# Optimization experiments

Measured on AMD Instinct MI355X. Metric: run time of the kernel, lower is better.

The kernel has to match this reference:

```python
import jax, jax.numpy as jnp
import numpy as np

QC = 12          # effective quantum channels (quantum_channels//4*4)
G = 3            # number of 4-channel quantum groups
DIM = 128
NGROUPS_GN = 8
NUM_LAYER = 1

# PauliZ sign table: wire 0 is the most-significant qubit (PennyLane default.qubit)
_SIGNS = np.array([[1.0 - 2.0 * ((k >> (3 - w)) & 1) for w in range(4)]
                   for k in range(16)], dtype=np.float32)


def _apply_rx(state, phi, w):
    # state: [B,2,2,2,2] complex64; phi: [B]; RX = cos(p/2) I - i sin(p/2) X
    c = jnp.cos(0.5 * phi).astype(jnp.complex64)
    s = (-1j) * jnp.sin(0.5 * phi).astype(jnp.complex64)
    U = jnp.stack([jnp.stack([c, s], -1), jnp.stack([s, c], -1)], -2)  # [B,2,2]
    st = jnp.moveaxis(state, 1 + w, -1)
    st = jnp.einsum('bij,b...j->b...i', U, st)
    return jnp.moveaxis(st, -1, 1 + w)


def _apply_cnot(state, c, t):
    st = jnp.moveaxis(state, (1 + c, 1 + t), (-2, -1))
    st = jnp.concatenate([st[..., 0:1, :], st[..., 1:2, ::-1]], axis=-2)
    return jnp.moveaxis(st, (-2, -1), (1 + c, 1 + t))


def _circuit(x4, theta):
    # AngleEmbedding(RX) + NUM_LAYER x Basic_ansatz; x4: [B,4], theta: [4*NUM_LAYER]
    B = x4.shape[0]
    state = jnp.zeros((B, 2, 2, 2, 2), jnp.complex64).at[:, 0, 0, 0, 0].set(1.0)
    for w in range(4):
        state = _apply_rx(state, x4[:, w], w)
    for l in range(NUM_LAYER):
        th = theta[4 * l:4 * (l + 1)]
        for w in range(4):
            state = _apply_rx(state, jnp.broadcast_to(th[w], (B,)), w)
        for c in range(3):
            state = _apply_cnot(state, c, c + 1)
        state = _apply_cnot(state, 3, 0)
    probs = jnp.abs(state.reshape(B, 16)) ** 2
    return probs @ jnp.asarray(_SIGNS)  # [B,4] PauliZ expvals


def _quantum_block(x_q, qparams):
    # x_q: [B,H,W,QC]; pool spatially, run per-group circuit, broadcast back
    B, H, W, Cq = x_q.shape
    pooled = jnp.mean(x_q, axis=(1, 2)).reshape(B, Cq // 4, 4)
    y = jax.vmap(_circuit, in_axes=(1, 0), out_axes=1)(pooled, qparams)  # [B,G,4]
    y = y.reshape(B, 1, 1, Cq)
    return jnp.broadcast_to(y, (B, H, W, Cq))


def _ws_conv(x, kernel, bias):
    eps = 1e-5  # fp32 branch of WeightStandardizedConv
    mean = jnp.mean(kernel, axis=(0, 1, 2), keepdims=True)
    var = jnp.var(kernel, axis=(0, 1, 2), keepdims=True)
    k = (kernel - mean) / jnp.sqrt(var + eps)
    y = jax.lax.conv_general_dilated(x, k, (1, 1), ((1, 1), (1, 1)),
                                     dimension_numbers=('NHWC', 'HWIO', 'NHWC'))
    return y + bias


def _group_norm(x, scale, bias, groups=NGROUPS_GN, eps=1e-6):
    B, H, W, C = x.shape
    xg = x.reshape(B, H, W, groups, C // groups)
    mu = jnp.mean(xg, axis=(1, 2, 4), keepdims=True)
    var = jnp.var(xg, axis=(1, 2, 4), keepdims=True)
    xn = ((xg - mu) / jnp.sqrt(var + eps)).reshape(B, H, W, C)
    return xn * scale + bias


def setup_inputs() -> dict:
    key = jax.random.key(0)
    ks = jax.random.split(key, 8)
    B, H, W, C, T = 16, 64, 64, DIM, 512
    cc = DIM - QC  # classical conv channels = 116
    return {
        'x': jax.random.normal(ks[0], (B, H, W, C), jnp.float32),
        'time_emb': jax.random.normal(ks[1], (B, T), jnp.float32),
        'qparams': jax.random.uniform(ks[2], (G, 4), jnp.float32),
        'conv0_kernel': jax.random.normal(ks[3], (3, 3, cc, cc), jnp.float32) * 0.05,
        'conv0_bias': jnp.zeros((cc,), jnp.float32),
        'conv1_kernel': jax.random.normal(ks[4], (3, 3, cc, cc), jnp.float32) * 0.05,
        'conv1_bias': jnp.zeros((cc,), jnp.float32),
        'gn0_scale': jnp.ones((C,), jnp.float32),
        'gn0_bias': jnp.zeros((C,), jnp.float32),
        'gn1_scale': jnp.ones((C,), jnp.float32),
        'gn1_bias': jnp.zeros((C,), jnp.float32),
        'time_w': jax.random.normal(ks[5], (T, 2 * DIM), jnp.float32) * 0.02,
        'time_b': jnp.zeros((2 * DIM,), jnp.float32),
    }


def reference(x, time_emb, qparams, conv0_kernel, conv0_bias, conv1_kernel,
              conv1_bias, gn0_scale, gn0_bias, gn1_scale, gn1_bias, time_w, time_b):
    # first quantum + classical branch
    h_q = _quantum_block(x[..., :QC], qparams)
    h_c = _ws_conv(x[..., QC:], conv0_kernel, conv0_bias)
    h = jnp.concatenate([h_q, h_c], axis=-1)
    h = _group_norm(h, gn0_scale, gn0_bias)
    # FiLM conditioning from time embedding
    t = jax.nn.swish(time_emb) @ time_w + time_b  # [B, 2*DIM]
    scale, shift = jnp.split(t[:, None, None, :], 2, axis=-1)
    h = jax.nn.swish(h * (1 + scale) + shift)
    # second quantum + classical branch
    h_q2 = _quantum_block(h[..., :QC], qparams)
    h_c2 = _ws_conv(h[..., QC:], conv1_kernel, conv1_bias)
    h2 = jnp.concatenate([h_q2, h_c2], axis=-1)
    h2 = jax.nn.swish(_group_norm(h2, gn1_scale, gn1_bias))
    return x + h2
```

## Files before the change

kernel.cpp:

```cpp
#include <hip/hip_runtime.h>
#include <math.h>

#define BATCH 16
#define NPX 4096
#define CDIM 128
#define CC 116
#define KTAPS 1044

using u16 = unsigned short;
typedef __attribute__((ext_vector_type(8))) short short8;
typedef __attribute__((ext_vector_type(16))) float f32x16;

__device__ __forceinline__ float swishf(float z) {
    return z / (1.f + __expf(-z));
}
__device__ __forceinline__ float bf2f(u16 u) {
    union { unsigned int i; float f; } v; v.i = ((unsigned int)u) << 16; return v.f;
}
__device__ __forceinline__ u16 f2bf(float f) {
    union { float f; unsigned int i; } v; v.f = f;
    unsigned int r = v.i + 0x7fffu + ((v.i >> 16) & 1u);
    return (u16)(r >> 16);
}
__device__ __forceinline__ unsigned cvtpk(float a, float b) {
    unsigned r;
    asm("v_cvt_pk_bf16_f32 %0, %1, %2" : "=v"(r) : "v"(a), "v"(b));
    return r;
}

__global__ void k_init(float* __restrict__ p) {
    int i = blockIdx.x * 256 + threadIdx.x;
    if (i < 8384) p[i] = 0.f;
}

__global__ void k_pool(const float* __restrict__ x, float* __restrict__ pooled) {
    int b = blockIdx.x;
    int tid = threadIdx.x;
    float s[12];
#pragma unroll
    for (int c = 0; c < 12; ++c) s[c] = 0.f;
    const float* xb = x + (size_t)b * NPX * CDIM;
    for (int px = tid; px < NPX; px += 256) {
        const float4* p = (const float4*)(xb + (size_t)px * CDIM);
        float4 v0 = p[0], v1 = p[1], v2 = p[2];
        s[0] += v0.x; s[1] += v0.y; s[2] += v0.z; s[3] += v0.w;
        s[4] += v1.x; s[5] += v1.y; s[6] += v1.z; s[7] += v1.w;
        s[8] += v2.x; s[9] += v2.y; s[10] += v2.z; s[11] += v2.w;
    }
    __shared__ float red[12][256];
#pragma unroll
    for (int c = 0; c < 12; ++c) red[c][tid] = s[c];
    __syncthreads();
    for (int st = 128; st > 0; st >>= 1) {
        if (tid < st) {
#pragma unroll
            for (int c = 0; c < 12; ++c) red[c][tid] += red[c][tid + st];
        }
        __syncthreads();
    }
    if (tid < 12) pooled[b * 12 + tid] = red[tid][0] * (1.f / 4096.f);
}

__device__ void run_circuit(const float* ang, const float* th, float* z) {
    float ar[16], ai[16];
#pragma unroll
    for (int k = 0; k < 16; ++k) { ar[k] = 0.f; ai[k] = 0.f; }
    ar[0] = 1.f;
#pragma unroll
    for (int pass = 0; pass < 2; ++pass) {
        const float* a = pass ? th : ang;
#pragma unroll
        for (int w = 0; w < 4; ++w) {
            float half = 0.5f * a[w];
            float cth = cosf(half), sth = sinf(half);
            int m = 1 << (3 - w);
#pragma unroll
            for (int k = 0; k < 16; ++k) {
                if (k & m) continue;
                int k2 = k | m;
                float r0 = ar[k], i0 = ai[k], r1 = ar[k2], i1 = ai[k2];
                ar[k]  = cth * r0 + sth * i1;
                ai[k]  = cth * i0 - sth * r1;
                ar[k2] = sth * i0 + cth * r1;
                ai[k2] = -sth * r0 + cth * i1;
            }
        }
    }
#pragma unroll
    for (int e = 0; e < 4; ++e) {
        const int cwi[4] = {0, 1, 2, 3};
        const int twi[4] = {1, 2, 3, 0};
        int mc = 1 << (3 - cwi[e]), mt = 1 << (3 - twi[e]);
#pragma unroll
        for (int k = 0; k < 16; ++k) {
            if ((k & mc) && !(k & mt)) {
                int k2 = k | mt;
                float tr = ar[k]; ar[k] = ar[k2]; ar[k2] = tr;
                float ti = ai[k]; ai[k] = ai[k2]; ai[k2] = ti;
            }
        }
    }
    float zz[4] = {0.f, 0.f, 0.f, 0.f};
#pragma unroll
    for (int k = 0; k < 16; ++k) {
        float p = ar[k] * ar[k] + ai[k] * ai[k];
#pragma unroll
        for (int w = 0; w < 4; ++w) zz[w] += ((k >> (3 - w)) & 1) ? -p : p;
    }
#pragma unroll
    for (int w = 0; w < 4; ++w) z[w] = zz[w];
}

__global__ void k_circ1(const float* __restrict__ pooled, const float* __restrict__ qp,
                        float* __restrict__ y1) {
    int tid = threadIdx.x;
    if (tid >= 48) return;
    int b = tid / 3, g = tid % 3;
    float z[4];
    run_circuit(pooled + b * 12 + g * 4, qp + g * 4, z);
#pragma unroll
    for (int w = 0; w < 4; ++w) y1[b * 12 + g * 4 + w] = z[w];
}

__global__ void k_time(const float* __restrict__ te, const float* __restrict__ W,
                       const float* __restrict__ tb, float* __restrict__ t) {
    int b = blockIdx.x, tid = threadIdx.x;
    __shared__ float se[512];
    for (int k = tid; k < 512; k += 256) {
        float z = te[b * 512 + k];
        se[k] = swishf(z);
    }
    __syncthreads();
    float acc = tb[tid];
    for (int k = 0; k < 512; ++k) acc += se[k] * W[k * 256 + tid];
    t[b * 256 + tid] = acc;
}

__global__ void k_wstd(const float* __restrict__ K0, const float* __restrict__ K1,
                       u16* __restrict__ kqp0, u16* __restrict__ kqp1) {
    const float* K = blockIdx.y ? K1 : K0;
    u16* kqp = blockIdx.y ? kqp1 : kqp0;
    int o = blockIdx.x;
    int tid = threadIdx.x;
    __shared__ float rs[256], rss[256];
    __shared__ float mb[2];
    float s = 0.f, ss = 0.f;
    if (o < CC) {
        for (int idx = tid; idx < KTAPS; idx += 256) {
            float v = K[(size_t)idx * CC + o];
            s += v; ss += v * v;
        }
    }
    rs[tid] = s; rss[tid] = ss;
    __syncthreads();
    for (int st = 128; st > 0; st >>= 1) {
        if (tid < st) { rs[tid] += rs[tid + st]; rss[tid] += rss[tid + st]; }
        __syncthreads();
    }
    if (tid == 0) {
        float m = rs[0] * (1.f / KTAPS);
        float var = rss[0] * (1.f / KTAPS) - m * m;
        mb[0] = m;
        mb[1] = rsqrtf(var + 1e-5f);
    }
    __syncthreads();
    float m = mb[0], inv = mb[1];
    for (int idx = tid; idx < 1152; idx += 256) {
        int tap = idx >> 7, ic = idx & 127;
        float v = 0.f;
        if (o < CC && ic < CC) v = (K[((size_t)tap * CC + ic) * CC + o] - m) * inv;
        int step = tap * 8 + (ic >> 4);
        int lane2 = ((ic >> 3) & 1) * 32 + (o & 31);
        int j = ic & 7;
        kqp[(size_t)(step * 4 + (o >> 5)) * 512 + lane2 * 8 + j] = f2bf(v);
    }
}

template <int MODE>
__launch_bounds__(256, 2)
__global__ void k_conv(const void* __restrict__ inp, const float* __restrict__ Acoef,
                       const float* __restrict__ Bcoef, const u16* __restrict__ kqp,
                       const float* __restrict__ bias, u16* __restrict__ outp,
                       float* __restrict__ csum) {
    __shared__ u16 As[4 * 64 * 128];
    const int hb = blockIdx.x;
    const int hp = ((hb & 7) << 2) | (hb >> 3);
    const int h0 = hp * 2;
    const int b = blockIdx.y;
    const int tid = threadIdx.x, lane = tid & 63, wid = tid >> 6;
    const int wm = wid & 1, wn = wid >> 1;
    const int pp = tid >> 2, ck = tid & 3;
    const int swz = (pp & 15) << 4;
    char* asb = (char*)As;

    float fr0[32], fr1[32], fr2[32], fr3[32];
    short8 sr0[4], sr1[4], sr2[4], sr3[4];
    bool val[4];

#define LOADROW(r, fv, sv)  do { \
    const int hi_ = h0 + (r) - 1; \
    val[r] = (hi_ >= 0 && hi_ < 64); \
    if (val[r]) { \
        const size_t px_ = (size_t)((b * 64 + hi_) * 64 + pp); \
        if (MODE == 0) { \
            const float* sp_ = (const float*)inp + px_ * 128 + 12 + ck * 32; \
            if (ck < 3) { \
                _Pragma("unroll") for (int j = 0; j < 8; ++j) *(float4*)&fv[j * 4] = ((const float4*)sp_)[j]; \
            } else { \
                _Pragma("unroll") for (int j = 0; j < 5; ++j) *(float4*)&fv[j * 4] = ((const float4*)sp_)[j]; \
                _Pragma("unroll") for (int e = 20; e < 32; ++e) fv[e] = 0.f; \
            } \
        } else { \
            const u16* sp_ = (const u16*)inp + px_ * 128 + ck * 32; \
            _Pragma("unroll") for (int k = 0; k < 4; ++k) sv[k] = ((const short8*)sp_)[k]; \
        } \
    } \
} while (0)

    LOADROW(0, fr0, sr0);
    LOADROW(1, fr1, sr1);
    LOADROW(2, fr2, sr2);
    LOADROW(3, fr3, sr3);

    float ca[32], cb[32];
    if (MODE == 1) {
        const float* ap = Acoef + b * 128 + 12 + ck * 32;
        const float* bpc = Bcoef + b * 128 + 12 + ck * 32;
        const int nj = (ck < 3) ? 8 : 5;
#pragma unroll
        for (int j = 0; j < 8; ++j)
            if (j < nj) {
                *(float4*)&ca[j * 4] = ((const float4*)ap)[j];
                *(float4*)&cb[j * 4] = ((const float4*)bpc)[j];
            }
        if (ck == 3) {
#pragma unroll
            for (int e = 20; e < 32; ++e) { ca[e] = 0.f; cb[e] = 0.f; }
        }
    }

    const u16* bp = kqp + ((size_t)(wn * 2) << 9) + ((size_t)lane << 3);
    short8 breg[3][2];
#pragma unroll
    for (int s = 0; s < 3; ++s) {
        breg[s][0] = *(const short8*)(bp + ((size_t)s << 11));
        breg[s][1] = *(const short8*)(bp + ((size_t)s << 11) + 512);
    }

#define WRITEROW(r, fv, sv) do { \
    unsigned pk_[16]; \
    if (val[r]) { \
        if (MODE == 0) { \
            _Pragma("unroll") for (int e = 0; e < 16; ++e) pk_[e] = cvtpk(fv[2 * e], fv[2 * e + 1]); \
        } else { \
            float g_[32]; \
            _Pragma("unroll") for (int e = 0; e < 32; ++e) { \
                float f_ = bf2f((u16)sv[e >> 3][e & 7]); \
                float w_ = swishf(f_ * ca[e] + cb[e]); \
                g_[e] = (e >= 20 && ck == 3) ? 0.f : w_; \
            } \
            _Pragma("unroll") for (int e = 0; e < 16; ++e) pk_[e] = cvtpk(g_[2 * e], g_[2 * e + 1]); \
        } \
    } else { \
        _Pragma("unroll") for (int e = 0; e < 16; ++e) pk_[e] = 0u; \
    } \
    char* rowb_ = asb + ((r) * 64 + pp) * 256; \
    _Pragma("unroll") for (int k = 0; k < 4; ++k) \
        *(short8*)(rowb_ + ((ck * 64 + k * 16) ^ swz)) = *(const short8*)&pk_[k * 4]; \
} while (0)

    const int l31 = lane & 31;
    const int chpart = (lane >> 5) << 4;
    int rowoff[3], swzv[3];
#pragma unroll
    for (int q = 0; q < 3; ++q) {
        int ppx = l31 + q - 1;
        int ppc = ppx < 0 ? 0 : ppx;
        rowoff[q] = ppc << 7;
        swzv[q] = (ppc & 15) << 4;
    }
    int rowoff1[3], swzv1[3];
#pragma unroll
    for (int q = 0; q < 3; ++q) {
        int ppx = 32 + l31 + q - 1;
        int ppc = ppx > 63 ? 63 : ppx;
        rowoff1[q] = ppc << 7;
        swzv1[q] = (ppc & 15) << 4;
    }
    const bool edge_lo = (l31 == 0);
    const bool edge_hi = (l31 == 31);
    const short8 zero8 = {0, 0, 0, 0, 0, 0, 0, 0};
    const u16* aw = As + wm * 8192;

    WRITEROW(0, fr0, sr0);
    WRITEROW(1, fr1, sr1);
    __syncthreads();

    f32x16 acc[2][2];
#pragma unroll
    for (int mf = 0; mf < 2; ++mf)
#pragma unroll
        for (int nf = 0; nf < 2; ++nf)
#pragma unroll
            for (int r = 0; r < 16; ++r) acc[mf][nf][r] = 0.f;

#define AREAD(dst, s) do { \
    const int tap_ = (s) >> 3, p2_ = tap_ / 3, q2_ = tap_ % 3; \
    const int cb2_ = ((s) & 7) << 5; \
    dst[0] = *(const short8*)&aw[p2_ * 8192 + rowoff[q2_] + (((cb2_ + chpart) ^ swzv[q2_]) >> 1)]; \
    dst[1] = *(const short8*)&aw[p2_ * 8192 + rowoff1[q2_] + (((cb2_ + chpart) ^ swzv1[q2_]) >> 1)]; \
} while (0)

#define DOSTEP(s, cur, nxt, lim) do { \
    const int slotB_ = (s) % 3; \
    if ((s) + 1 < (lim)) AREAD(afrag[nxt], (s) + 1); \
    const int q_ = ((s) >> 3) % 3; \
    short8 a0_ = afrag[cur][0], a1_ = afrag[cur][1]; \
    if (q_ == 0) a0_ = edge_lo ? zero8 : a0_; \
    if (q_ == 2) a1_ = edge_hi ? zero8 : a1_; \
    __builtin_amdgcn_s_setprio(1); \
    acc[0][0] = __builtin_amdgcn_mfma_f32_32x32x16_bf16(a0_, breg[slotB_][0], acc[0][0], 0, 0, 0); \
    acc[0][1] = __builtin_amdgcn_mfma_f32_32x32x16_bf16(a0_, breg[slotB_][1], acc[0][1], 0, 0, 0); \
    acc[1][0] = __builtin_amdgcn_mfma_f32_32x32x16_bf16(a1_, breg[slotB_][0], acc[1][0], 0, 0, 0); \
    acc[1][1] = __builtin_amdgcn_mfma_f32_32x32x16_bf16(a1_, breg[slotB_][1], acc[1][1], 0, 0, 0); \
    __builtin_amdgcn_s_setprio(0); \
    if ((s) + 3 < 72) { \
        breg[slotB_][0] = *(const short8*)(bp + ((size_t)((s) + 3) << 11)); \
        breg[slotB_][1] = *(const short8*)(bp + ((size_t)((s) + 3) << 11) + 512); \
    } \
} while (0)

    short8 afrag[2][2];
    AREAD(afrag[0], 0);
#pragma unroll
    for (int s = 0; s < 24; ++s) {
        const int cur = s & 1, nxt = cur ^ 1;
        DOSTEP(s, cur, nxt, 24);
    }

    WRITEROW(2, fr2, sr2);
    WRITEROW(3, fr3, sr3);
    __syncthreads();

    AREAD(afrag[0], 24);
#pragma unroll
    for (int s = 24; s < 72; ++s) {
        const int cur = (s - 24) & 1, nxt = cur ^ 1;
        DOSTEP(s, cur, nxt, 72);
    }

    float bv[2], cs[2], cq[2];
#pragma unroll
    for (int nf = 0; nf < 2; ++nf) {
        int oc = wn * 64 + nf * 32 + l31;
        bv[nf] = (oc < CC) ? bias[oc] : 0.f;
        cs[nf] = 0.f; cq[nf] = 0.f;
    }
    const int rbase = (lane >> 5) * 4;
    size_t obase = (size_t)(b * 4096 + (h0 + wm) * 64) * 128;
#pragma unroll
    for (int mf = 0; mf < 2; ++mf)
#pragma unroll
        for (int nf = 0; nf < 2; ++nf) {
            int oc = wn * 64 + nf * 32 + l31;
#pragma unroll
            for (int r = 0; r < 16; ++r) {
                int row = (r & 3) + ((r >> 2) << 3) + rbase;
                int px = mf * 32 + row;
                float v = acc[mf][nf][r] + bv[nf];
                outp[obase + (size_t)px * 128 + oc] = (u16)cvtpk(v, v);
                cs[nf] += v;
                cq[nf] += v * v;
            }
        }
#pragma unroll
    for (int nf = 0; nf < 2; ++nf) {
        cs[nf] += __shfl_xor(cs[nf], 32);
        cq[nf] += __shfl_xor(cq[nf], 32);
        if (lane < 32) {
            int oc = wn * 64 + nf * 32 + l31;
            atomicAdd(&csum[(b * 128 + oc) * 2], cs[nf]);
            atomicAdd(&csum[(b * 128 + oc) * 2 + 1], cq[nf]);
        }
    }
#undef LOADROW
#undef WRITEROW
#undef AREAD
#undef DOSTEP
}

__global__ void k_mid0(const float* __restrict__ csum, const float* __restrict__ y1,
                       const float* __restrict__ t, const float* __restrict__ gs,
                       const float* __restrict__ gb, const float* __restrict__ qp,
                       float* __restrict__ A, float* __restrict__ Bc,
                       float* __restrict__ y2) {
    __shared__ float sst[128][2];
    int tid = threadIdx.x;
    if (tid < 128) {
        int b = tid >> 3, g = tid & 7;
        float S = 0.f, SS = 0.f;
#pragma unroll
        for (int e = 0; e < 16; ++e) {
            int orig = g * 16 + e;
            if (orig >= 12) {
                int cc = orig - 12;
                S += csum[(b * 128 + cc) * 2];
                SS += csum[(b * 128 + cc) * 2 + 1];
            }
        }
        if (g == 0) {
#pragma unroll
            for (int c = 0; c < 12; ++c) {
                float v = y1[b * 12 + c];
                S += 4096.f * v;
                SS += 4096.f * v * v;
            }
        }
        float mu = S * (1.f / 65536.f);
        float var = SS * (1.f / 65536.f) - mu * mu;
        sst[tid][0] = mu;
        sst[tid][1] = rsqrtf(var + 1e-6f);
    }
    __syncthreads();
    for (int i = tid; i < 2048; i += 256) {
        int b = i >> 7, c = i & 127, g = c >> 4;
        float mu = sst[b * 8 + g][0], isd = sst[b * 8 + g][1];
        float sc = t[b * 256 + c], sh = t[b * 256 + 128 + c];
        float a = isd * gs[c];
        float bb = gb[c] - mu * a;
        A[i] = a * (1.f + sc);
        Bc[i] = bb * (1.f + sc) + sh;
    }
    if (tid < 48) {
        int b = tid / 3, gq = tid % 3;
        float pin[4], z[4];
        float mu = sst[b * 8][0], isd = sst[b * 8][1];
#pragma unroll
        for (int w = 0; w < 4; ++w) {
            int c = gq * 4 + w;
            float a = isd * gs[c];
            float bb = gb[c] - mu * a;
            float sc = t[b * 256 + c], sh = t[b * 256 + 128 + c];
            float v = y1[b * 12 + c];
            pin[w] = swishf(v * (a * (1.f + sc)) + (bb * (1.f + sc) + sh));
        }
        run_circuit(pin, qp + gq * 4, z);
#pragma unroll
        for (int w = 0; w < 4; ++w) y2[b * 12 + gq * 4 + w] = z[w];
    }
}

__global__ void k_mid1(const float* __restrict__ csum, const float* __restrict__ y2,
                       const float* __restrict__ gs, const float* __restrict__ gb,
                       float* __restrict__ A2, float* __restrict__ B2,
                       float* __restrict__ oq) {
    __shared__ float sst[128][2];
    int tid = threadIdx.x;
    if (tid < 128) {
        int b = tid >> 3, g = tid & 7;
        float S = 0.f, SS = 0.f;
#pragma unroll
        for (int e = 0; e < 16; ++e) {
            int orig = g * 16 + e;
            if (orig >= 12) {
                int cc = orig - 12;
                S += csum[(b * 128 + cc) * 2];
                SS += csum[(b * 128 + cc) * 2 + 1];
            }
        }
        if (g == 0) {
#pragma unroll
            for (int c = 0; c < 12; ++c) {
                float v = y2[b * 12 + c];
                S += 4096.f * v;
                SS += 4096.f * v * v;
            }
        }
        float mu = S * (1.f / 65536.f);
        float var = SS * (1.f / 65536.f) - mu * mu;
        sst[tid][0] = mu;
        sst[tid][1] = rsqrtf(var + 1e-6f);
    }
    __syncthreads();
    for (int i = tid; i < 2048; i += 256) {
        int b = i >> 7, c = i & 127, g = c >> 4;
        float mu = sst[b * 8 + g][0], isd = sst[b * 8 + g][1];
        float a = isd * gs[c];
        A2[i] = a;
        B2[i] = gb[c] - mu * a;
    }
    if (tid < 192) {
        int b = tid / 12, c = tid % 12;
        float mu = sst[b * 8][0], isd = sst[b * 8][1];
        float a = isd * gs[c];
        float bb = gb[c] - mu * a;
        oq[b * 12 + c] = swishf(y2[b * 12 + c] * a + bb);
    }
}

__global__ void k_final(const float* __restrict__ x, const u16* __restrict__ co,
                        const float* __restrict__ A2, const float* __restrict__ B2,
                        const float* __restrict__ oq, float* __restrict__ outp) {
    const int t = blockIdx.x, b = blockIdx.y;
    const int seg = t >> 6, hraw = t & 63;
    const int h = ((hraw & 7) << 3) | (hraw >> 3);
    const int tid = threadIdx.x;
    const size_t px = (size_t)(b * 64 + h) * 64 + seg * 8 + (tid >> 5);
    const int c4 = tid & 31, c = c4 * 4;
    float4 xv = *(const float4*)(x + px * CDIM + c);
    float4 r;
    if (c4 < 3) {
        const float* q = oq + b * 12 + c;
        r.x = xv.x + q[0]; r.y = xv.y + q[1]; r.z = xv.z + q[2]; r.w = xv.w + q[3];
    } else {
        int cc = c - 12;
        const u16* hp = co + px * 128 + cc;
        float4 a = *(const float4*)(A2 + b * 128 + c);
        float4 bb = *(const float4*)(B2 + b * 128 + c);
        r.x = xv.x + swishf(bf2f(hp[0]) * a.x + bb.x);
        r.y = xv.y + swishf(bf2f(hp[1]) * a.y + bb.y);
        r.z = xv.z + swishf(bf2f(hp[2]) * a.z + bb.z);
        r.w = xv.w + swishf(bf2f(hp[3]) * a.w + bb.w);
    }
    *(float4*)(outp + px * CDIM + c) = r;
}

extern "C" void kernel_launch(void* const* d_in, const int* in_sizes, int n_in,
                              void* d_out, int out_size, void* d_ws, size_t ws_size,
                              hipStream_t stream) {
    const float* x        = (const float*)d_in[0];
    const float* time_emb = (const float*)d_in[1];
    const float* qparams  = (const float*)d_in[2];
    const float* c0k      = (const float*)d_in[3];
    const float* c0b      = (const float*)d_in[4];
    const float* c1k      = (const float*)d_in[5];
    const float* c1b      = (const float*)d_in[6];
    const float* g0s      = (const float*)d_in[7];
    const float* g0b      = (const float*)d_in[8];
    const float* g1s      = (const float*)d_in[9];
    const float* g1b      = (const float*)d_in[10];
    const float* tw       = (const float*)d_in[11];
    const float* tb       = (const float*)d_in[12];
    float* outp = (float*)d_out;
    float* ws = (float*)d_ws;

    size_t o = 0;
    auto alloc = [&](size_t n) { size_t r = o; o += (n + 15) & ~(size_t)15; return r; };
    float* zbase  = ws + alloc(8384);
    float* pooled = zbase;
    float* csum0  = zbase + 192;
    float* csum1  = zbase + 192 + 4096;
    float* y1     = ws + alloc(192);
    float* y2     = ws + alloc(192);
    float* t      = ws + alloc(4096);
    float* A      = ws + alloc(2048);
    float* Bc     = ws + alloc(2048);
    float* A2     = ws + alloc(2048);
    float* B2     = ws + alloc(2048);
    float* oq     = ws + alloc(192);
    u16* kqp0     = (u16*)(ws + alloc(73728));
    u16* kqp1     = (u16*)(ws + alloc(73728));
    u16* convA    = (u16*)(ws + alloc(4194304));
    u16* convB    = (u16*)(ws + alloc(4194304));

    k_init<<<33, 256, 0, stream>>>(zbase);
    k_pool<<<16, 256, 0, stream>>>(x, pooled);
    k_time<<<16, 256, 0, stream>>>(time_emb, tw, tb, t);
    k_wstd<<<dim3(128, 2), 256, 0, stream>>>(c0k, c1k, kqp0, kqp1);
    k_circ1<<<1, 64, 0, stream>>>(pooled, qparams, y1);

    dim3 cgrid(32, 16);
    k_conv<0><<<cgrid, 256, 0, stream>>>(x, nullptr, nullptr, kqp0, c0b, convA, csum0);
    k_mid0<<<1, 256, 0, stream>>>(csum0, y1, t, g0s, g0b, qparams, A, Bc, y2);

    k_conv<1><<<cgrid, 256, 0, stream>>>(convA, A, Bc, kqp1, c1b, convB, csum1);
    k_mid1<<<1, 256, 0, stream>>>(csum1, y2, g1s, g1b, A2, B2, oq);
    k_final<<<dim3(512, 16), 256, 0, stream>>>(x, convB, A2, B2, oq, outp);
}
```

Measured before the change: 129.9 us.

## Widen conv blocks to 512 threads, stage output via LDS, merge small prologue kernels

The conv kernel now runs 512 threads per block. Each wave computes a 64x32 output tile instead of 64x64, which cuts accumulator and staging registers so more waves fit per CU. Output is staged through shared memory so global stores become coalesced 16-byte writes, and the FiLM coefficients move into shared memory. The prologue launches (init, pool, time, weight-standardize, circuit) are merged into two kernels, with the pool split across more blocks and the first circuit folded into k_mid0. The trade-off is more barriers and scalar bf16 conversion in place of packed cvt instructions.

```diff
diff --git a/kernel.cpp b/kernel.cpp
--- a/kernel.cpp
+++ b/kernel.cpp
@@ -22,26 +22,24 @@
     unsigned int r = v.i + 0x7fffu + ((v.i >> 16) & 1u);
     return (u16)(r >> 16);
 }
-__device__ __forceinline__ unsigned cvtpk(float a, float b) {
-    unsigned r;
-    asm("v_cvt_pk_bf16_f32 %0, %1, %2" : "=v"(r) : "v"(a), "v"(b));
-    return r;
-}
-
-__global__ void k_init(float* __restrict__ p) {
-    int i = blockIdx.x * 256 + threadIdx.x;
-    if (i < 8384) p[i] = 0.f;
-}
-
-__global__ void k_pool(const float* __restrict__ x, float* __restrict__ pooled) {
-    int b = blockIdx.x;
-    int tid = threadIdx.x;
+
+__global__ void k_pre(const float* __restrict__ x, float* __restrict__ part,
+                      float* __restrict__ csums) {
+    const int bx = blockIdx.x, tid = threadIdx.x;
+    if (bx >= 128) {
+        int i = (bx - 128) * 256 + tid;
+        csums[i * 2] = 0.f;
+        csums[i * 2 + 1] = 0.f;
+        return;
+    }
+    const int b = bx >> 3, seg = bx & 7;
     float s[12];
 #pragma unroll
     for (int c = 0; c < 12; ++c) s[c] = 0.f;
-    const float* xb = x + (size_t)b * NPX * CDIM;
-    for (int px = tid; px < NPX; px += 256) {
-        const float4* p = (const float4*)(xb + (size_t)px * CDIM);
+    const float* xb = x + (size_t)(b * 4096 + seg * 512) * CDIM;
+#pragma unroll
+    for (int i = 0; i < 2; ++i) {
+        const float4* p = (const float4*)(xb + (size_t)(tid + i * 256) * CDIM);
         float4 v0 = p[0], v1 = p[1], v2 = p[2];
         s[0] += v0.x; s[1] += v0.y; s[2] += v0.z; s[3] += v0.w;
         s[4] += v1.x; s[5] += v1.y; s[6] += v1.z; s[7] += v1.w;
@@ -58,7 +56,7 @@
         }
         __syncthreads();
     }
-    if (tid < 12) pooled[b * 12 + tid] = red[tid][0] * (1.f / 4096.f);
+    if (tid < 12) part[bx * 12 + tid] = red[tid][0];
 }
 
 __device__ void run_circuit(const float* ang, const float* th, float* z) {
@@ -111,39 +109,26 @@
     for (int w = 0; w < 4; ++w) z[w] = zz[w];
 }
 
-__global__ void k_circ1(const float* __restrict__ pooled, const float* __restrict__ qp,
-                        float* __restrict__ y1) {
-    int tid = threadIdx.x;
-    if (tid >= 48) return;
-    int b = tid / 3, g = tid % 3;
-    float z[4];
-    run_circuit(pooled + b * 12 + g * 4, qp + g * 4, z);
-#pragma unroll
-    for (int w = 0; w < 4; ++w) y1[b * 12 + g * 4 + w] = z[w];
-}
-
-__global__ void k_time(const float* __restrict__ te, const float* __restrict__ W,
-                       const float* __restrict__ tb, float* __restrict__ t) {
-    int b = blockIdx.x, tid = threadIdx.x;
+__global__ void k_tw(const float* __restrict__ te, const float* __restrict__ W,
+                     const float* __restrict__ tb, float* __restrict__ t,
+                     const float* __restrict__ K0, const float* __restrict__ K1,
+                     u16* __restrict__ kqp0, u16* __restrict__ kqp1) {
+    const int bx = blockIdx.x, tid = threadIdx.x;
     __shared__ float se[512];
-    for (int k = tid; k < 512; k += 256) {
-        float z = te[b * 512 + k];
-        se[k] = swishf(z);
-    }
-    __syncthreads();
-    float acc = tb[tid];
-    for (int k = 0; k < 512; ++k) acc += se[k] * W[k * 256 + tid];
-    t[b * 256 + tid] = acc;
-}
-
-__global__ void k_wstd(const float* __restrict__ K0, const float* __restrict__ K1,
-                       u16* __restrict__ kqp0, u16* __restrict__ kqp1) {
-    const float* K = blockIdx.y ? K1 : K0;
-    u16* kqp = blockIdx.y ? kqp1 : kqp0;
-    int o = blockIdx.x;
-    int tid = threadIdx.x;
-    __shared__ float rs[256], rss[256];
-    __shared__ float mb[2];
+    __shared__ float rs[256], rss[256], mb[2];
+    if (bx < 16) {
+        const int b = bx;
+        for (int k = tid; k < 512; k += 256) se[k] = swishf(te[b * 512 + k]);
+        __syncthreads();
+        float acc = tb[tid];
+        for (int k = 0; k < 512; ++k) acc += se[k] * W[k * 256 + tid];
+        t[b * 256 + tid] = acc;
+        return;
+    }
+    const int r = bx - 16;
+    const float* K = (r >> 7) ? K1 : K0;
+    u16* kqp = (r >> 7) ? kqp1 : kqp0;
+    const int o = r & 127;
     float s = 0.f, ss = 0.f;
     if (o < CC) {
         for (int idx = tid; idx < KTAPS; idx += 256) {
@@ -177,30 +162,35 @@
 }
 
 template <int MODE>
-__launch_bounds__(256, 2)
+__launch_bounds__(512, 4)
 __global__ void k_conv(const void* __restrict__ inp, const float* __restrict__ Acoef,
                        const float* __restrict__ Bcoef, const u16* __restrict__ kqp,
                        const float* __restrict__ bias, u16* __restrict__ outp,
                        float* __restrict__ csum) {
-    __shared__ u16 As[4 * 64 * 128];
-    const int hb = blockIdx.x;
+    __shared__ u16 As[32768];
+    __shared__ float cf[256];
+    const int hb = blockIdx.x, b = blockIdx.y;
     const int hp = ((hb & 7) << 2) | (hb >> 3);
     const int h0 = hp * 2;
-    const int b = blockIdx.y;
     const int tid = threadIdx.x, lane = tid & 63, wid = tid >> 6;
     const int wm = wid & 1, wn = wid >> 1;
-    const int pp = tid >> 2, ck = tid & 3;
+    const int l31 = lane & 31;
+    const int rr = tid >> 8, pp = (tid >> 2) & 63, ck = tid & 3;
     const int swz = (pp & 15) << 4;
-    char* asb = (char*)As;
-
-    float fr0[32], fr1[32], fr2[32], fr3[32];
-    short8 sr0[4], sr1[4], sr2[4], sr3[4];
-    bool val[4];
-
-#define LOADROW(r, fv, sv)  do { \
+
+    if (MODE == 1) {
+        if (tid < 128) {
+            cf[tid] = Acoef[b * 128 + tid];
+            cf[128 + tid] = Bcoef[b * 128 + tid];
+        }
+    }
+
+    float fv[32]; short8 sv[4];
+
+#define LOADCHUNK(r, val) do { \
     const int hi_ = h0 + (r) - 1; \
-    val[r] = (hi_ >= 0 && hi_ < 64); \
-    if (val[r]) { \
+    val = (hi_ >= 0 && hi_ < 64); \
+    if (val) { \
         const size_t px_ = (size_t)((b * 64 + hi_) * 64 + pp); \
         if (MODE == 0) { \
             const float* sp_ = (const float*)inp + px_ * 128 + 12 + ck * 32; \
@@ -217,185 +207,157 @@
     } \
 } while (0)
 
-    LOADROW(0, fr0, sr0);
-    LOADROW(1, fr1, sr1);
-    LOADROW(2, fr2, sr2);
-    LOADROW(3, fr3, sr3);
-
-    float ca[32], cb[32];
-    if (MODE == 1) {
-        const float* ap = Acoef + b * 128 + 12 + ck * 32;
-        const float* bpc = Bcoef + b * 128 + 12 + ck * 32;
-        const int nj = (ck < 3) ? 8 : 5;
-#pragma unroll
-        for (int j = 0; j < 8; ++j)
-            if (j < nj) {
-                *(float4*)&ca[j * 4] = ((const float4*)ap)[j];
-                *(float4*)&cb[j * 4] = ((const float4*)bpc)[j];
-            }
-        if (ck == 3) {
-#pragma unroll
-            for (int e = 20; e < 32; ++e) { ca[e] = 0.f; cb[e] = 0.f; }
-        }
-    }
-
-    const u16* bp = kqp + ((size_t)(wn * 2) << 9) + ((size_t)lane << 3);
-    short8 breg[3][2];
-#pragma unroll
-    for (int s = 0; s < 3; ++s) {
-        breg[s][0] = *(const short8*)(bp + ((size_t)s << 11));
-        breg[s][1] = *(const short8*)(bp + ((size_t)s << 11) + 512);
-    }
-
-#define WRITEROW(r, fv, sv) do { \
-    unsigned pk_[16]; \
-    if (val[r]) { \
+#define WRITECHUNK(r, val) do { \
+    u16 t_[32]; \
+    if (val) { \
         if (MODE == 0) { \
-            _Pragma("unroll") for (int e = 0; e < 16; ++e) pk_[e] = cvtpk(fv[2 * e], fv[2 * e + 1]); \
+            _Pragma("unroll") for (int e = 0; e < 32; ++e) t_[e] = f2bf(fv[e]); \
         } else { \
-            float g_[32]; \
             _Pragma("unroll") for (int e = 0; e < 32; ++e) { \
-                float f_ = bf2f((u16)sv[e >> 3][e & 7]); \
-                float w_ = swishf(f_ * ca[e] + cb[e]); \
-                g_[e] = (e >= 20 && ck == 3) ? 0.f : w_; \
+                int c_ = ck * 32 + e; \
+                if (c_ < CC) { \
+                    float f_ = bf2f((u16)sv[e >> 3][e & 7]); \
+                    t_[e] = f2bf(swishf(f_ * cf[12 + c_] + cf[140 + c_])); \
+                } else t_[e] = 0; \
             } \
-            _Pragma("unroll") for (int e = 0; e < 16; ++e) pk_[e] = cvtpk(g_[2 * e], g_[2 * e + 1]); \
         } \
     } else { \
-        _Pragma("unroll") for (int e = 0; e < 16; ++e) pk_[e] = 0u; \
+        _Pragma("unroll") for (int e = 0; e < 32; ++e) t_[e] = 0; \
     } \
-    char* rowb_ = asb + ((r) * 64 + pp) * 256; \
+    char* rb_ = (char*)As + ((r) * 64 + pp) * 256; \
     _Pragma("unroll") for (int k = 0; k < 4; ++k) \
-        *(short8*)(rowb_ + ((ck * 64 + k * 16) ^ swz)) = *(const short8*)&pk_[k * 4]; \
+        *(short8*)(rb_ + ((ck * 64 + k * 16) ^ swz)) = *(const short8*)&t_[k * 8]; \
 } while (0)
 
-    const int l31 = lane & 31;
-    const int chpart = (lane >> 5) << 4;
-    int rowoff[3], swzv[3];
-#pragma unroll
-    for (int q = 0; q < 3; ++q) {
-        int ppx = l31 + q - 1;
-        int ppc = ppx < 0 ? 0 : ppx;
-        rowoff[q] = ppc << 7;
-        swzv[q] = (ppc & 15) << 4;
-    }
-    int rowoff1[3], swzv1[3];
-#pragma unroll
-    for (int q = 0; q < 3; ++q) {
-        int ppx = 32 + l31 + q - 1;
-        int ppc = ppx > 63 ? 63 : ppx;
-        rowoff1[q] = ppc << 7;
-        swzv1[q] = (ppc & 15) << 4;
-    }
-    const bool edge_lo = (l31 == 0);
-    const bool edge_hi = (l31 == 31);
+    bool valA, valC;
+    LOADCHUNK(rr, valA);
+    if (MODE == 1) __syncthreads();
+    WRITECHUNK(rr, valA);
+    LOADCHUNK(2 + rr, valC);
+
+    const u16* bp = kqp + (size_t)wn * 512 + (size_t)lane * 8;
+    short8 breg[4];
+#pragma unroll
+    for (int s = 0; s < 4; ++s) breg[s] = *(const short8*)(bp + ((size_t)s << 11));
+
+    const int kh16 = (lane >> 5) << 4;
+    int coloff[2][3], colswz[2][3];
+#pragma unroll
+    for (int mf = 0; mf < 2; ++mf)
+#pragma unroll
+        for (int q = 0; q < 3; ++q) {
+            int c = mf * 32 + l31 + q - 1;
+            int cc = c < 0 ? 0 : (c > 63 ? 63 : c);
+            coloff[mf][q] = cc << 7;
+            colswz[mf][q] = (cc & 15) << 4;
+        }
+    const bool e0 = (l31 == 0), e1 = (l31 == 31);
     const short8 zero8 = {0, 0, 0, 0, 0, 0, 0, 0};
-    const u16* aw = As + wm * 8192;
-
-    WRITEROW(0, fr0, sr0);
-    WRITEROW(1, fr1, sr1);
-    __syncthreads();
-
-    f32x16 acc[2][2];
+    const int rowb = wm * 8192;
+
+    asm volatile("s_waitcnt lgkmcnt(0)" ::: "memory");
+    __builtin_amdgcn_s_barrier();
+
+    f32x16 acc[2];
 #pragma unroll
     for (int mf = 0; mf < 2; ++mf)
 #pragma unroll
-        for (int nf = 0; nf < 2; ++nf)
-#pragma unroll
-            for (int r = 0; r < 16; ++r) acc[mf][nf][r] = 0.f;
+        for (int r = 0; r < 16; ++r) acc[mf][r] = 0.f;
 
 #define AREAD(dst, s) do { \
-    const int tap_ = (s) >> 3, p2_ = tap_ / 3, q2_ = tap_ % 3; \
-    const int cb2_ = ((s) & 7) << 5; \
-    dst[0] = *(const short8*)&aw[p2_ * 8192 + rowoff[q2_] + (((cb2_ + chpart) ^ swzv[q2_]) >> 1)]; \
-    dst[1] = *(const short8*)&aw[p2_ * 8192 + rowoff1[q2_] + (((cb2_ + chpart) ^ swzv1[q2_]) >> 1)]; \
+    const int tap_ = (s) >> 3, p_ = tap_ / 3, q_ = tap_ % 3; \
+    const int chb_ = ((s) & 7) << 5; \
+    dst[0] = *(const short8*)&As[rowb + p_ * 8192 + coloff[0][q_] + (((chb_ + kh16) ^ colswz[0][q_]) >> 1)]; \
+    dst[1] = *(const short8*)&As[rowb + p_ * 8192 + coloff[1][q_] + (((chb_ + kh16) ^ colswz[1][q_]) >> 1)]; \
 } while (0)
 
-#define DOSTEP(s, cur, nxt, lim) do { \
-    const int slotB_ = (s) % 3; \
-    if ((s) + 1 < (lim)) AREAD(afrag[nxt], (s) + 1); \
+#define STEP(s, base, lim) do { \
+    const int cur_ = ((s) - (base)) & 1, nxt_ = cur_ ^ 1; \
+    if ((s) + 1 < (lim)) AREAD(afr[nxt_], (s) + 1); \
     const int q_ = ((s) >> 3) % 3; \
-    short8 a0_ = afrag[cur][0], a1_ = afrag[cur][1]; \
-    if (q_ == 0) a0_ = edge_lo ? zero8 : a0_; \
-    if (q_ == 2) a1_ = edge_hi ? zero8 : a1_; \
-    __builtin_amdgcn_s_setprio(1); \
-    acc[0][0] = __builtin_amdgcn_mfma_f32_32x32x16_bf16(a0_, breg[slotB_][0], acc[0][0], 0, 0, 0); \
-    acc[0][1] = __builtin_amdgcn_mfma_f32_32x32x16_bf16(a0_, breg[slotB_][1], acc[0][1], 0, 0, 0); \
-    acc[1][0] = __builtin_amdgcn_mfma_f32_32x32x16_bf16(a1_, breg[slotB_][0], acc[1][0], 0, 0, 0); \
-    acc[1][1] = __builtin_amdgcn_mfma_f32_32x32x16_bf16(a1_, breg[slotB_][1], acc[1][1], 0, 0, 0); \
-    __builtin_amdgcn_s_setprio(0); \
-    if ((s) + 3 < 72) { \
-        breg[slotB_][0] = *(const short8*)(bp + ((size_t)((s) + 3) << 11)); \
-        breg[slotB_][1] = *(const short8*)(bp + ((size_t)((s) + 3) << 11) + 512); \
-    } \
+    short8 a0_ = afr[cur_][0], a1_ = afr[cur_][1]; \
+    if (q_ == 0) a0_ = e0 ? zero8 : a0_; \
+    if (q_ == 2) a1_ = e1 ? zero8 : a1_; \
+    acc[0] = __builtin_amdgcn_mfma_f32_32x32x16_bf16(a0_, breg[(s) & 3], acc[0], 0, 0, 0); \
+    acc[1] = __builtin_amdgcn_mfma_f32_32x32x16_bf16(a1_, breg[(s) & 3], acc[1], 0, 0, 0); \
+    if ((s) + 4 < 72) breg[(s) & 3] = *(const short8*)(bp + ((size_t)((s) + 4) << 11)); \
 } while (0)
 
-    short8 afrag[2][2];
-    AREAD(afrag[0], 0);
-#pragma unroll
-    for (int s = 0; s < 24; ++s) {
-        const int cur = s & 1, nxt = cur ^ 1;
-        DOSTEP(s, cur, nxt, 24);
-    }
-
-    WRITEROW(2, fr2, sr2);
-    WRITEROW(3, fr3, sr3);
-    __syncthreads();
-
-    AREAD(afrag[0], 24);
-#pragma unroll
-    for (int s = 24; s < 72; ++s) {
-        const int cur = (s - 24) & 1, nxt = cur ^ 1;
-        DOSTEP(s, cur, nxt, 72);
-    }
-
-    float bv[2], cs[2], cq[2];
-#pragma unroll
-    for (int nf = 0; nf < 2; ++nf) {
-        int oc = wn * 64 + nf * 32 + l31;
-        bv[nf] = (oc < CC) ? bias[oc] : 0.f;
-        cs[nf] = 0.f; cq[nf] = 0.f;
-    }
-    const int rbase = (lane >> 5) * 4;
-    size_t obase = (size_t)(b * 4096 + (h0 + wm) * 64) * 128;
-#pragma unroll
-    for (int mf = 0; mf < 2; ++mf)
-#pragma unroll
-        for (int nf = 0; nf < 2; ++nf) {
-            int oc = wn * 64 + nf * 32 + l31;
-#pragma unroll
-            for (int r = 0; r < 16; ++r) {
-                int row = (r & 3) + ((r >> 2) << 3) + rbase;
-                int px = mf * 32 + row;
-                float v = acc[mf][nf][r] + bv[nf];
-                outp[obase + (size_t)px * 128 + oc] = (u16)cvtpk(v, v);
-                cs[nf] += v;
-                cq[nf] += v * v;
-            }
-        }
-#pragma unroll
-    for (int nf = 0; nf < 2; ++nf) {
-        cs[nf] += __shfl_xor(cs[nf], 32);
-        cq[nf] += __shfl_xor(cq[nf], 32);
-        if (lane < 32) {
-            int oc = wn * 64 + nf * 32 + l31;
-            atomicAdd(&csum[(b * 128 + oc) * 2], cs[nf]);
-            atomicAdd(&csum[(b * 128 + oc) * 2 + 1], cq[nf]);
-        }
-    }
-#undef LOADROW
-#undef WRITEROW
+    short8 afr[2][2];
+    AREAD(afr[0], 0);
+#pragma unroll
+    for (int s = 0; s < 24; ++s) STEP(s, 0, 24);
+
+    WRITECHUNK(2 + rr, valC);
+    asm volatile("s_waitcnt lgkmcnt(0)" ::: "memory");
+    __builtin_amdgcn_s_barrier();
+
+    AREAD(afr[0], 24);
+#pragma unroll
+    for (int s = 24; s < 72; ++s) STEP(s, 24, 72);
+
+    const int oc = wn * 32 + l31;
+    const float bv = (oc < CC) ? bias[oc] : 0.f;
+    float cs = 0.f, cq = 0.f;
+    const int rbase = (lane >> 5) << 2;
+
+    asm volatile("s_waitcnt lgkmcnt(0)" ::: "memory");
+    __builtin_amdgcn_s_barrier();
+#pragma unroll
+    for (int mf = 0; mf < 2; ++mf) {
+#pragma unroll
+        for (int r = 0; r < 16; ++r) {
+            int drow = (r & 3) + ((r >> 2) << 3) + rbase;
+            int flat = wm * 64 + mf * 32 + drow;
+            float v = acc[mf][r] + bv;
+            As[flat * 128 + oc] = f2bf(v);
+            cs += v;
+            cq += v * v;
+        }
+    }
+    asm volatile("s_waitcnt lgkmcnt(0)" ::: "memory");
+    __builtin_amdgcn_s_barrier();
+    {
+        size_t obase = (size_t)(b * 4096 + h0 * 64) * 128;
+#pragma unroll
+        for (int k = 0; k < 4; ++k)
+            *(short8*)&outp[obase + k * 4096 + tid * 8] = *(const short8*)&As[k * 4096 + tid * 8];
+    }
+    cs += __shfl_xor(cs, 32);
+    cq += __shfl_xor(cq, 32);
+    if (lane < 32) {
+        atomicAdd(&csum[(b * 128 + oc) * 2], cs);
+        atomicAdd(&csum[(b * 128 + oc) * 2 + 1], cq);
+    }
+#undef LOADCHUNK
+#undef WRITECHUNK
 #undef AREAD
-#undef DOSTEP
-}
-
-__global__ void k_mid0(const float* __restrict__ csum, const float* __restrict__ y1,
+#undef STEP
+}
+
+__global__ void k_mid0(const float* __restrict__ part, const float* __restrict__ csum,
                        const float* __restrict__ t, const float* __restrict__ gs,
                        const float* __restrict__ gb, const float* __restrict__ qp,
                        float* __restrict__ A, float* __restrict__ Bc,
                        float* __restrict__ y2) {
-    __shared__ float sst[128][2];
+    __shared__ float pooled_s[192], y1s[192], sst[128][2];
     int tid = threadIdx.x;
+    if (tid < 192) {
+        int b = tid / 12, c = tid % 12;
+        float s = 0.f;
+#pragma unroll
+        for (int k = 0; k < 8; ++k) s += part[(b * 8 + k) * 12 + c];
+        pooled_s[tid] = s * (1.f / 4096.f);
+    }
+    __syncthreads();
+    if (tid < 48) {
+        int b = tid / 3, g = tid % 3;
+        float z[4];
+        run_circuit(&pooled_s[b * 12 + g * 4], qp + g * 4, z);
+#pragma unroll
+        for (int w = 0; w < 4; ++w) y1s[b * 12 + g * 4 + w] = z[w];
+    }
+    __syncthreads();
     if (tid < 128) {
         int b = tid >> 3, g = tid & 7;
         float S = 0.f, SS = 0.f;
@@ -411,7 +373,7 @@
         if (g == 0) {
 #pragma unroll
             for (int c = 0; c < 12; ++c) {
-                float v = y1[b * 12 + c];
+                float v = y1s[b * 12 + c];
                 S += 4096.f * v;
                 SS += 4096.f * v * v;
             }
@@ -441,7 +403,7 @@
             float a = isd * gs[c];
             float bb = gb[c] - mu * a;
             float sc = t[b * 256 + c], sh = t[b * 256 + 128 + c];
-            float v = y1[b * 12 + c];
+            float v = y1s[b * 12 + c];
             pin[w] = swishf(v * (a * (1.f + sc)) + (bb * (1.f + sc) + sh));
         }
         run_circuit(pin, qp + gq * 4, z);
@@ -546,34 +508,30 @@
 
     size_t o = 0;
     auto alloc = [&](size_t n) { size_t r = o; o += (n + 15) & ~(size_t)15; return r; };
-    float* zbase  = ws + alloc(8384);
-    float* pooled = zbase;
-    float* csum0  = zbase + 192;
-    float* csum1  = zbase + 192 + 4096;
-    float* y1     = ws + alloc(192);
-    float* y2     = ws + alloc(192);
+    float* part   = ws + alloc(1536);
+    float* csums  = ws + alloc(8192);
+    float* csum0  = csums;
+    float* csum1  = csums + 4096;
     float* t      = ws + alloc(4096);
     float* A      = ws + alloc(2048);
     float* Bc     = ws + alloc(2048);
     float* A2     = ws + alloc(2048);
     float* B2     = ws + alloc(2048);
+    float* y2     = ws + alloc(192);
     float* oq     = ws + alloc(192);
     u16* kqp0     = (u16*)(ws + alloc(73728));
     u16* kqp1     = (u16*)(ws + alloc(73728));
     u16* convA    = (u16*)(ws + alloc(4194304));
     u16* convB    = (u16*)(ws + alloc(4194304));
 
-    k_init<<<33, 256, 0, stream>>>(zbase);
-    k_pool<<<16, 256, 0, stream>>>(x, pooled);
-    k_time<<<16, 256, 0, stream>>>(time_emb, tw, tb, t);
-    k_wstd<<<dim3(128, 2), 256, 0, stream>>>(c0k, c1k, kqp0, kqp1);
-    k_circ1<<<1, 64, 0, stream>>>(pooled, qparams, y1);
+    k_pre<<<144, 256, 0, stream>>>(x, part, csums);
+    k_tw<<<272, 256, 0, stream>>>(time_emb, tw, tb, t, c0k, c1k, kqp0, kqp1);
 
     dim3 cgrid(32, 16);
-    k_conv<0><<<cgrid, 256, 0, stream>>>(x, nullptr, nullptr, kqp0, c0b, convA, csum0);
-    k_mid0<<<1, 256, 0, stream>>>(csum0, y1, t, g0s, g0b, qparams, A, Bc, y2);
-
-    k_conv<1><<<cgrid, 256, 0, stream>>>(convA, A, Bc, kqp1, c1b, convB, csum1);
+    k_conv<0><<<cgrid, 512, 0, stream>>>(x, nullptr, nullptr, kqp0, c0b, convA, csum0);
+    k_mid0<<<1, 256, 0, stream>>>(part, csum0, t, g0s, g0b, qparams, A, Bc, y2);
+
+    k_conv<1><<<cgrid, 512, 0, stream>>>(convA, A, Bc, kqp1, c1b, convB, csum1);
     k_mid1<<<1, 256, 0, stream>>>(csum1, y2, g1s, g1b, A2, B2, oq);
     k_final<<<dim3(512, 16), 256, 0, stream>>>(x, convB, A2, B2, oq, outp);
 }
```

After: 127.2 us. 1.02x faster.
